# Performance work log

Hardware: AMD Instinct MI355X
Metric: run time of the kernel (lower is better)

## Reference

```python
import jax, jax.numpy as jnp
import numpy as np

N_NODES = 50000
N_EDGES = 300000
IN_FEATS = 1433
HIDDEN = 16
OUT_FEATS = 7


def setup_inputs() -> dict:
    key = jax.random.key(0)
    k1, k2, k3, k4, k5, k6, k7, k8 = jax.random.split(key, 8)
    features = jax.random.normal(k1, (N_NODES, IN_FEATS), dtype=jnp.float32)
    src = jax.random.randint(k2, (N_EDGES,), 0, N_NODES, dtype=jnp.int32)
    dst = jax.random.randint(k3, (N_EDGES,), 0, N_NODES, dtype=jnp.int32)
    # Linear layer params (PyTorch default-ish init scale)
    s1 = 1.0 / np.sqrt(IN_FEATS)
    s2 = 1.0 / np.sqrt(HIDDEN)
    W1 = jax.random.uniform(k4, (IN_FEATS, HIDDEN), jnp.float32, -s1, s1)
    b1 = jax.random.uniform(k5, (HIDDEN,), jnp.float32, -s1, s1)
    W2 = jax.random.uniform(k6, (HIDDEN, OUT_FEATS), jnp.float32, -s2, s2)
    b2 = jax.random.uniform(k7, (OUT_FEATS,), jnp.float32, -s2, s2)
    return {"features": features, "src": src, "dst": dst,
            "W1": W1, "b1": b1, "W2": W2, "b2": b2}


def _gcn_layer(h, src, dst, W, b):
    # copy_src message + sum reduce + self term: h'_v = sum_{u->v} h_u + h_v
    agg = jax.ops.segment_sum(h[src], dst, num_segments=N_NODES) + h
    return agg @ W + b


def reference(features, src, dst, W1, b1, W2, b2):
    x = jax.nn.relu(_gcn_layer(features, src, dst, W1, b1))
    # dropout is identity in eval mode
    x = _gcn_layer(x, src, dst, W2, b2)
    return x
```

## Files before the change

### kernel.cpp

```cpp
#include <hip/hip_runtime.h>
#include <hip/hip_fp16.h>

#define N_NODES  50000
#define N_EDGES  300000
#define IN_FEATS 1433
#define HIDDEN   16
#define OUT_F    7
#define KPAD     1472
#define WROW     9

__global__ __launch_bounds__(256) void k1_gemm(
    const float* __restrict__ F, const float* __restrict__ W1,
    const float* __restrict__ b1, __half* __restrict__ H,
    __half* __restrict__ aggbuf)
{
    __shared__ unsigned int Wl[KPAD * WROW];
    const int tid = threadIdx.x;

    for (int idx = tid; idx < KPAD * 8; idx += 256) {
        int k = idx >> 3, c = idx & 7;
        unsigned int u = 0u;
        if (k < IN_FEATS) {
            __half2 h2 = __floats2half2_rn(W1[k * 16 + 2 * c], W1[k * 16 + 2 * c + 1]);
            u = *reinterpret_cast<unsigned int*>(&h2);
        }
        Wl[k * WROW + c] = u;
    }
    __syncthreads();

    const int lane = tid & 63;
    const float b1v = b1[lane & 15];
    const int gwave  = blockIdx.x * 4 + (tid >> 6);
    const int nwaves = gridDim.x * 4;

    for (int ch = gwave; ch < N_NODES / 4; ch += nwaves) {
        const int r0 = ch * 4;
        const float* fp = F + (size_t)r0 * IN_FEATS;

        float v[64];
        #pragma unroll
        for (int i = 0; i < 64; ++i) v[i] = 0.f;

        #pragma unroll 2
        for (int i = 0; i < 22; ++i) {
            const int k = i * 64 + lane;
            const float f0 = fp[k];
            const float f1 = fp[IN_FEATS + k];
            const float f2 = fp[2 * IN_FEATS + k];
            const float f3 = fp[3 * IN_FEATS + k];
            float wv[16];
            #pragma unroll
            for (int c = 0; c < 8; ++c) {
                unsigned int u = Wl[k * WROW + c];
                __half2 h2 = *reinterpret_cast<__half2*>(&u);
                float2 f = __half22float2(h2);
                wv[2 * c]     = f.x;
                wv[2 * c + 1] = f.y;
            }
            #pragma unroll
            for (int j = 0; j < 16; ++j) {
                v[j]      += f0 * wv[j];
                v[16 + j] += f1 * wv[j];
                v[32 + j] += f2 * wv[j];
                v[48 + j] += f3 * wv[j];
            }
        }
        {
            const int k = 1408 + lane;
            float f0 = 0.f, f1 = 0.f, f2 = 0.f, f3 = 0.f;
            if (k < IN_FEATS) {
                f0 = fp[k];
                f1 = fp[IN_FEATS + k];
                f2 = fp[2 * IN_FEATS + k];
                f3 = fp[3 * IN_FEATS + k];
            }
            float wv[16];
            #pragma unroll
            for (int c = 0; c < 8; ++c) {
                unsigned int u = Wl[k * WROW + c];
                __half2 h2 = *reinterpret_cast<__half2*>(&u);
                float2 f = __half22float2(h2);
                wv[2 * c]     = f.x;
                wv[2 * c + 1] = f.y;
            }
            #pragma unroll
            for (int j = 0; j < 16; ++j) {
                v[j]      += f0 * wv[j];
                v[16 + j] += f1 * wv[j];
                v[32 + j] += f2 * wv[j];
                v[48 + j] += f3 * wv[j];
            }
        }

        #pragma unroll
        for (int d = 5; d >= 0; --d) {
            const int half = 1 << d;
            const bool hi = (lane >> d) & 1;
            #pragma unroll
            for (int t = 0; t < (1 << d); ++t) {
                float sent = hi ? v[t] : v[t + half];
                float recv = __shfl_xor(sent, half, 64);
                float keep = hi ? v[t + half] : v[t];
                v[t] = keep + recv;
            }
        }
        const size_t off = (size_t)r0 * 16 + lane;
        H[off]      = __float2half(v[0]);
        aggbuf[off] = __float2half(v[0] + b1v);
    }
}

__global__ __launch_bounds__(256) void k2_scatter1(
    const int* __restrict__ src, const int* __restrict__ dst,
    const __half2* __restrict__ H2, __half2* __restrict__ agg2)
{
    int t = blockIdx.x * 256 + threadIdx.x;
    int e = t >> 3, p = t & 7;
    int s = src[e], d = dst[e];
    __half2 val = H2[(size_t)s * 8 + p];
    unsafeAtomicAdd(&agg2[(size_t)d * 8 + p], val);
}

__global__ __launch_bounds__(256) void k3_layer2(
    const __half2* __restrict__ agg2, const float* __restrict__ W2,
    const float* __restrict__ b2, float* __restrict__ G,
    float* __restrict__ out)
{
    int n = blockIdx.x * 256 + threadIdx.x;
    if (n >= N_NODES) return;
    float x[16];
    #pragma unroll
    for (int p = 0; p < 8; ++p) {
        float2 f = __half22float2(agg2[(size_t)n * 8 + p]);
        x[2 * p]     = f.x > 0.f ? f.x : 0.f;
        x[2 * p + 1] = f.y > 0.f ? f.y : 0.f;
    }
    #pragma unroll
    for (int j = 0; j < OUT_F; ++j) {
        float g = 0.f;
        #pragma unroll
        for (int k = 0; k < 16; ++k) g += x[k] * W2[k * OUT_F + j];
        G[(size_t)n * OUT_F + j] = g;
        out[(size_t)n * OUT_F + j] = g + b2[j];
    }
}

__global__ __launch_bounds__(256) void k4_scatter2(
    const int* __restrict__ src, const int* __restrict__ dst,
    const float* __restrict__ G, float* __restrict__ out)
{
    int t = blockIdx.x * 256 + threadIdx.x;
    int e = t / OUT_F, j = t % OUT_F;
    if (e < N_EDGES) {
        atomicAdd(&out[(size_t)dst[e] * OUT_F + j], G[(size_t)src[e] * OUT_F + j]);
    }
}

extern "C" void kernel_launch(void* const* d_in, const int* in_sizes, int n_in,
                              void* d_out, int out_size, void* d_ws, size_t ws_size,
                              hipStream_t stream)
{
    const float* F   = (const float*)d_in[0];
    const int*   src = (const int*)d_in[1];
    const int*   dst = (const int*)d_in[2];
    const float* W1  = (const float*)d_in[3];
    const float* b1  = (const float*)d_in[4];
    const float* W2  = (const float*)d_in[5];
    const float* b2  = (const float*)d_in[6];
    float* out = (float*)d_out;

    __half* H      = (__half*)d_ws;
    __half* aggbuf = H + (size_t)N_NODES * HIDDEN;
    float*  G      = (float*)(aggbuf + (size_t)N_NODES * HIDDEN);

    k1_gemm<<<768, 256, 0, stream>>>(F, W1, b1, H, aggbuf);
    k2_scatter1<<<(N_EDGES * 8) / 256, 256, 0, stream>>>(src, dst,
        (const __half2*)H, (__half2*)aggbuf);
    k3_layer2<<<(N_NODES + 255) / 256, 256, 0, stream>>>((const __half2*)aggbuf,
        W2, b2, G, out);
    k4_scatter2<<<(N_EDGES * OUT_F + 255) / 256, 256, 0, stream>>>(src, dst, G, out);
}
```

Baseline: 116.8 us.

## Use MFMA for first GEMM and packed fp16 atomics in second scatter

Replaces the scalar FMA layer-1 GEMM, with its LDS-staged weights and shuffle reduction, by an MFMA 16x16x32 f16 kernel. A new pre-pack kernel lays out W1 in fragment order for it. The second layer now keeps its per-node 7-wide messages in padded half8 rows, scatters them with packed half2 atomics instead of fp32 atomics, and adds a final conversion kernel back to fp32 output. The aim is to cut GEMM compute and atomic traffic, at the cost of two extra launches, more fp16 accumulation error in the output, and uncoalesced per-lane 8-float loads of F.

```diff
diff --git a/kernel.cpp b/kernel.cpp
--- a/kernel.cpp
+++ b/kernel.cpp
@@ -6,107 +6,73 @@
 #define IN_FEATS 1433
 #define HIDDEN   16
 #define OUT_F    7
-#define KPAD     1472
-#define WROW     9
+#define NSTEP    45
+#define NCHUNK   3125
 
-__global__ __launch_bounds__(256) void k1_gemm(
-    const float* __restrict__ F, const float* __restrict__ W1,
+typedef __attribute__((ext_vector_type(8))) _Float16 f16x8;
+typedef __attribute__((ext_vector_type(4))) float    f32x4;
+
+__global__ __launch_bounds__(256) void k0_pack(const float* __restrict__ W1,
+                                               __half* __restrict__ Wb)
+{
+    int t = blockIdx.x * 256 + threadIdx.x;
+    int s = t >> 9, rem = t & 511, l = rem >> 3, i = rem & 7;
+    int k = s * 32 + ((l >> 4) << 3) + i, n = l & 15;
+    float v = (k < IN_FEATS) ? W1[k * 16 + n] : 0.f;
+    Wb[t] = __float2half(v);
+}
+
+__global__ __launch_bounds__(256) void k1_mfma(
+    const float* __restrict__ F, const __half* __restrict__ Wb,
     const float* __restrict__ b1, __half* __restrict__ H,
     __half* __restrict__ aggbuf)
 {
-    __shared__ unsigned int Wl[KPAD * WROW];
     const int tid = threadIdx.x;
+    const int wid = blockIdx.x * 4 + (tid >> 6);
+    if (wid >= NCHUNK) return;
+    const int lane = tid & 63;
+    const int m  = lane & 15;
+    const int kg = lane >> 4;
+    const int r0 = wid * 16;
+    const float* fa = F + (size_t)(r0 + m) * IN_FEATS + kg * 8;
+    const f16x8* Wf = (const f16x8*)Wb;
 
-    for (int idx = tid; idx < KPAD * 8; idx += 256) {
-        int k = idx >> 3, c = idx & 7;
-        unsigned int u = 0u;
-        if (k < IN_FEATS) {
-            __half2 h2 = __floats2half2_rn(W1[k * 16 + 2 * c], W1[k * 16 + 2 * c + 1]);
-            u = *reinterpret_cast<unsigned int*>(&h2);
-        }
-        Wl[k * WROW + c] = u;
+    f32x4 acc = {0.f, 0.f, 0.f, 0.f};
+
+    #pragma unroll 4
+    for (int s = 0; s < NSTEP - 1; ++s) {
+        const float* p = fa + s * 32;
+        f16x8 av;
+        av[0] = (_Float16)p[0]; av[1] = (_Float16)p[1];
+        av[2] = (_Float16)p[2]; av[3] = (_Float16)p[3];
+        av[4] = (_Float16)p[4]; av[5] = (_Float16)p[5];
+        av[6] = (_Float16)p[6]; av[7] = (_Float16)p[7];
+        f16x8 bv = Wf[s * 64 + lane];
+        acc = __builtin_amdgcn_mfma_f32_16x16x32_f16(av, bv, acc, 0, 0, 0);
     }
-    __syncthreads();
+    {
+        const float* p = fa + 44 * 32;
+        const bool hi = (kg == 3);
+        f16x8 av;
+        av[0] = (_Float16)p[0];
+        av[1] = (_Float16)(hi ? 0.f : p[1]);
+        av[2] = (_Float16)(hi ? 0.f : p[2]);
+        av[3] = (_Float16)(hi ? 0.f : p[3]);
+        av[4] = (_Float16)(hi ? 0.f : p[4]);
+        av[5] = (_Float16)(hi ? 0.f : p[5]);
+        av[6] = (_Float16)(hi ? 0.f : p[6]);
+        av[7] = (_Float16)(hi ? 0.f : p[7]);
+        f16x8 bv = Wf[44 * 64 + lane];
+        acc = __builtin_amdgcn_mfma_f32_16x16x32_f16(av, bv, acc, 0, 0, 0);
+    }
 
-    const int lane = tid & 63;
-    const float b1v = b1[lane & 15];
-    const int gwave  = blockIdx.x * 4 + (tid >> 6);
-    const int nwaves = gridDim.x * 4;
-
-    for (int ch = gwave; ch < N_NODES / 4; ch += nwaves) {
-        const int r0 = ch * 4;
-        const float* fp = F + (size_t)r0 * IN_FEATS;
-
-        float v[64];
-        #pragma unroll
-        for (int i = 0; i < 64; ++i) v[i] = 0.f;
-
-        #pragma unroll 2
-        for (int i = 0; i < 22; ++i) {
-            const int k = i * 64 + lane;
-            const float f0 = fp[k];
-            const float f1 = fp[IN_FEATS + k];
-            const float f2 = fp[2 * IN_FEATS + k];
-            const float f3 = fp[3 * IN_FEATS + k];
-            float wv[16];
-            #pragma unroll
-            for (int c = 0; c < 8; ++c) {
-                unsigned int u = Wl[k * WROW + c];
-                __half2 h2 = *reinterpret_cast<__half2*>(&u);
-                float2 f = __half22float2(h2);
-                wv[2 * c]     = f.x;
-                wv[2 * c + 1] = f.y;
-            }
-            #pragma unroll
-            for (int j = 0; j < 16; ++j) {
-                v[j]      += f0 * wv[j];
-                v[16 + j] += f1 * wv[j];
-                v[32 + j] += f2 * wv[j];
-                v[48 + j] += f3 * wv[j];
-            }
-        }
-        {
-            const int k = 1408 + lane;
-            float f0 = 0.f, f1 = 0.f, f2 = 0.f, f3 = 0.f;
-            if (k < IN_FEATS) {
-                f0 = fp[k];
-                f1 = fp[IN_FEATS + k];
-                f2 = fp[2 * IN_FEATS + k];
-                f3 = fp[3 * IN_FEATS + k];
-            }
-            float wv[16];
-            #pragma unroll
-            for (int c = 0; c < 8; ++c) {
-                unsigned int u = Wl[k * WROW + c];
-                __half2 h2 = *reinterpret_cast<__half2*>(&u);
-                float2 f = __half22float2(h2);
-                wv[2 * c]     = f.x;
-                wv[2 * c + 1] = f.y;
-            }
-            #pragma unroll
-            for (int j = 0; j < 16; ++j) {
-                v[j]      += f0 * wv[j];
-                v[16 + j] += f1 * wv[j];
-                v[32 + j] += f2 * wv[j];
-                v[48 + j] += f3 * wv[j];
-            }
-        }
-
-        #pragma unroll
-        for (int d = 5; d >= 0; --d) {
-            const int half = 1 << d;
-            const bool hi = (lane >> d) & 1;
-            #pragma unroll
-            for (int t = 0; t < (1 << d); ++t) {
-                float sent = hi ? v[t] : v[t + half];
-                float recv = __shfl_xor(sent, half, 64);
-                float keep = hi ? v[t + half] : v[t];
-                v[t] = keep + recv;
-            }
-        }
-        const size_t off = (size_t)r0 * 16 + lane;
-        H[off]      = __float2half(v[0]);
-        aggbuf[off] = __float2half(v[0] + b1v);
+    const float bj = b1[m];
+    #pragma unroll
+    for (int i = 0; i < 4; ++i) {
+        const int row = r0 + kg * 4 + i;
+        const float v = acc[i];
+        H[(size_t)row * 16 + m]      = __float2half(v);
+        aggbuf[(size_t)row * 16 + m] = __float2half(v + bj);
     }
 }
 
@@ -117,14 +83,13 @@
     int t = blockIdx.x * 256 + threadIdx.x;
     int e = t >> 3, p = t & 7;
     int s = src[e], d = dst[e];
-    __half2 val = H2[(size_t)s * 8 + p];
-    unsafeAtomicAdd(&agg2[(size_t)d * 8 + p], val);
+    unsafeAtomicAdd(&agg2[(size_t)d * 8 + p], H2[(size_t)s * 8 + p]);
 }
 
 __global__ __launch_bounds__(256) void k3_layer2(
     const __half2* __restrict__ agg2, const float* __restrict__ W2,
-    const float* __restrict__ b2, float* __restrict__ G,
-    float* __restrict__ out)
+    const float* __restrict__ b2, __half* __restrict__ Gh,
+    __half* __restrict__ oacc)
 {
     int n = blockIdx.x * 256 + threadIdx.x;
     if (n >= N_NODES) return;
@@ -135,25 +100,45 @@
         x[2 * p]     = f.x > 0.f ? f.x : 0.f;
         x[2 * p + 1] = f.y > 0.f ? f.y : 0.f;
     }
+    float g[8], o[8];
     #pragma unroll
-    for (int j = 0; j < OUT_F; ++j) {
-        float g = 0.f;
+    for (int j = 0; j < 7; ++j) {
+        float s = 0.f;
         #pragma unroll
-        for (int k = 0; k < 16; ++k) g += x[k] * W2[k * OUT_F + j];
-        G[(size_t)n * OUT_F + j] = g;
-        out[(size_t)n * OUT_F + j] = g + b2[j];
+        for (int k = 0; k < 16; ++k) s += x[k] * W2[k * OUT_F + j];
+        g[j] = s;
+        o[j] = s + b2[j];
     }
+    g[7] = 0.f; o[7] = 0.f;
+
+    union U { uint4 u; __half2 h[4]; };
+    U gu, ou;
+    #pragma unroll
+    for (int p = 0; p < 4; ++p) {
+        gu.h[p] = __floats2half2_rn(g[2 * p], g[2 * p + 1]);
+        ou.h[p] = __floats2half2_rn(o[2 * p], o[2 * p + 1]);
+    }
+    *(uint4*)(Gh   + (size_t)n * 8) = gu.u;
+    *(uint4*)(oacc + (size_t)n * 8) = ou.u;
 }
 
 __global__ __launch_bounds__(256) void k4_scatter2(
     const int* __restrict__ src, const int* __restrict__ dst,
-    const float* __restrict__ G, float* __restrict__ out)
+    const __half2* __restrict__ Gh2, __half2* __restrict__ oacc2)
 {
     int t = blockIdx.x * 256 + threadIdx.x;
-    int e = t / OUT_F, j = t % OUT_F;
-    if (e < N_EDGES) {
-        atomicAdd(&out[(size_t)dst[e] * OUT_F + j], G[(size_t)src[e] * OUT_F + j]);
-    }
+    if (t >= N_EDGES * 4) return;
+    int e = t >> 2, p = t & 3;
+    unsafeAtomicAdd(&oacc2[(size_t)dst[e] * 4 + p], Gh2[(size_t)src[e] * 4 + p]);
+}
+
+__global__ __launch_bounds__(256) void k5_out(
+    const __half* __restrict__ oacc, float* __restrict__ out)
+{
+    int t = blockIdx.x * 256 + threadIdx.x;
+    if (t >= N_NODES * OUT_F) return;
+    int n = t / 7, j = t - n * 7;
+    out[t] = __half2float(oacc[(size_t)n * 8 + j]);
 }
 
 extern "C" void kernel_launch(void* const* d_in, const int* in_sizes, int n_in,
@@ -169,14 +154,19 @@
     const float* b2  = (const float*)d_in[6];
     float* out = (float*)d_out;
 
-    __half* H      = (__half*)d_ws;
-    __half* aggbuf = H + (size_t)N_NODES * HIDDEN;
-    float*  G      = (float*)(aggbuf + (size_t)N_NODES * HIDDEN);
+    __half* H    = (__half*)d_ws;
+    __half* agg  = H + (size_t)N_NODES * HIDDEN;
+    __half* Wb   = agg + (size_t)N_NODES * HIDDEN;
+    __half* Gh   = Wb + NSTEP * 512;
+    __half* oacc = Gh + (size_t)N_NODES * 8;
 
-    k1_gemm<<<768, 256, 0, stream>>>(F, W1, b1, H, aggbuf);
+    k0_pack<<<(NSTEP * 512) / 256, 256, 0, stream>>>(W1, Wb);
+    k1_mfma<<<(NCHUNK + 3) / 4, 256, 0, stream>>>(F, Wb, b1, H, agg);
     k2_scatter1<<<(N_EDGES * 8) / 256, 256, 0, stream>>>(src, dst,
-        (const __half2*)H, (__half2*)aggbuf);
-    k3_layer2<<<(N_NODES + 255) / 256, 256, 0, stream>>>((const __half2*)aggbuf,
-        W2, b2, G, out);
-    k4_scatter2<<<(N_EDGES * OUT_F + 255) / 256, 256, 0, stream>>>(src, dst, G, out);
+        (const __half2*)H, (__half2*)agg);
+    k3_layer2<<<(N_NODES + 255) / 256, 256, 0, stream>>>((const __half2*)agg,
+        W2, b2, Gh, oacc);
+    k4_scatter2<<<(N_EDGES * 4 + 255) / 256, 256, 0, stream>>>(src, dst,
+        (const __half2*)Gh, (__half2*)oacc);
+    k5_out<<<(N_NODES * OUT_F + 255) / 256, 256, 0, stream>>>(oacc, out);
 }
```

Measured after the change: 122.4 us. 1.05x slower.
